# Performance work log

Hardware: AMD Instinct MI355X
Metric: run time of the kernel (lower is better)

The kernel has to match this reference:

```python
import jax, jax.numpy as jnp
import numpy as np

D = 2048      # input_dim
E = 16        # num_experts
H = 1024      # expert_units
K = 4         # k_top
B = 4096      # batch


def setup_inputs() -> dict:
    key = jax.random.key(0)
    ks = jax.random.split(key, 7)
    s1 = 1.0 / np.sqrt(D)
    s2 = 1.0 / np.sqrt(H)
    return {
        "x": jax.random.normal(ks[0], (B, D), dtype=jnp.float32),
        "W1": jax.random.uniform(ks[1], (E, D, H), jnp.float32, -s1, s1),
        "b1": jax.random.uniform(ks[2], (E, H), jnp.float32, -s1, s1),
        "W2": jax.random.uniform(ks[3], (E, H, D), jnp.float32, -s2, s2),
        "b2": jax.random.uniform(ks[4], (E, D), jnp.float32, -s2, s2),
        "Wr": jax.random.uniform(ks[5], (D, E), jnp.float32, -s1, s1),
        "br": jax.random.uniform(ks[6], (E,), jnp.float32, -s1, s1),
    }


def reference(x, W1, b1, W2, b2, Wr, br):
    # Router + top-k (torch.topk returns sorted descending; lax.top_k matches)
    logits = x @ Wr + br                          # [B, E]
    top_w, top_i = jax.lax.top_k(logits, K)       # [B, K]
    top_w = jax.nn.softmax(top_w, axis=1)

    # Dense all-expert MLP (eval mode: dropout is identity)
    h = jax.nn.relu(jnp.einsum('bd,edh->beh', x, W1) + b1)   # [B, E, H]
    expert_out = jnp.einsum('beh,ehd->bed', h, W2) + b2      # [B, E, D]

    # mask/detach trick: forward value is unchanged (identity in fwd)
    mask = jax.nn.one_hot(top_i, E, dtype=expert_out.dtype).sum(axis=1)  # [B, E]
    m = mask[:, :, None]
    expert_out = expert_out * m + jax.lax.stop_gradient(expert_out * (1.0 - m))

    # Gather top-k experts and combine
    sel = jnp.take_along_axis(expert_out, top_i[:, :, None], axis=1)    # [B, K, D]
    out = (sel * top_w[:, :, None]).sum(axis=1)
    return out + x
```

## Files before the change

kernel.cpp:

```cpp
#include <hip/hip_runtime.h>
#include <math.h>

#define D_   2048
#define E_   16
#define H_   1024
#define KSEL 4
#define B_   4096
#define CAP  4096

typedef short bf16x8_t __attribute__((ext_vector_type(8)));
typedef float f32x4_t  __attribute__((ext_vector_type(4)));

__device__ __forceinline__ unsigned short f2bf(float f) {
  unsigned u = __float_as_uint(f);
  u += 0x7FFFu + ((u >> 16) & 1u);
  return (unsigned short)(u >> 16);
}

__device__ __forceinline__ float bf2f(unsigned short h) {
  unsigned u = (unsigned)h << 16;
  return __uint_as_float(u);
}

__device__ __forceinline__ void gld16(const void* g, void* l) {
  __builtin_amdgcn_global_load_lds(
      (const __attribute__((address_space(1))) unsigned int*)g,
      (__attribute__((address_space(3))) unsigned int*)l, 16, 0, 0);
}

__global__ __launch_bounds__(256) void k_prepw(
    const float* __restrict__ Wr, float* __restrict__ wrT,
    const float* __restrict__ W1, unsigned short* __restrict__ W1t,
    const float* __restrict__ W2, unsigned short* __restrict__ W2t) {
  __shared__ float tile[64][65];
  int b = blockIdx.x;
  int w = threadIdx.x;
  if (b < 128) {
    int i = b * 256 + w;
    int d = i >> 4, e = i & 15;
    wrT[e * D_ + d] = Wr[i];
    return;
  }
  int g0 = (b - 128) * 2;
  const float* src[2]; unsigned short* dst[2];
  int RR[2], CC[2], r0t[2], c0t[2];
#pragma unroll
  for (int tt = 0; tt < 2; tt++) {
    int g = g0 + tt;
    if (g < 8192) {
      int e = g >> 9, rem = g & 511;
      src[tt] = W1 + (size_t)e * D_ * H_;
      dst[tt] = W1t + (size_t)e * D_ * H_;
      RR[tt] = 2048; CC[tt] = 1024;
      r0t[tt] = (rem >> 4) * 64; c0t[tt] = (rem & 15) * 64;
    } else {
      int g2 = g - 8192;
      int e = g2 >> 9, rem = g2 & 511;
      src[tt] = W2 + (size_t)e * D_ * H_;
      dst[tt] = W2t + (size_t)e * D_ * H_;
      RR[tt] = 1024; CC[tt] = 2048;
      r0t[tt] = (rem >> 5) * 64; c0t[tt] = (rem & 31) * 64;
    }
  }
  int cf4 = w & 15, rr = w >> 4;
  float4 v0[4], v1[4];
#pragma unroll
  for (int p = 0; p < 4; p++)
    v0[p] = *(const float4*)(src[0] + (size_t)(r0t[0] + p * 16 + rr) * CC[0] + c0t[0] + cf4 * 4);
#pragma unroll
  for (int p = 0; p < 4; p++)
    v1[p] = *(const float4*)(src[1] + (size_t)(r0t[1] + p * 16 + rr) * CC[1] + c0t[1] + cf4 * 4);
#pragma unroll
  for (int p = 0; p < 4; p++) {
    int r = p * 16 + rr;
    tile[r][cf4 * 4 + 0] = v0[p].x;
    tile[r][cf4 * 4 + 1] = v0[p].y;
    tile[r][cf4 * 4 + 2] = v0[p].z;
    tile[r][cf4 * 4 + 3] = v0[p].w;
  }
  __syncthreads();
#pragma unroll
  for (int it = 0; it < 8; it++) {
    int idx = it * 256 + w;
    int i = idx >> 5, rp = idx & 31;
    ushort2 v;
    v.x = f2bf(tile[2 * rp][i]);
    v.y = f2bf(tile[2 * rp + 1][i]);
    *(ushort2*)(dst[0] + (size_t)(c0t[0] + i) * RR[0] + r0t[0] + 2 * rp) = v;
  }
  __syncthreads();
#pragma unroll
  for (int p = 0; p < 4; p++) {
    int r = p * 16 + rr;
    tile[r][cf4 * 4 + 0] = v1[p].x;
    tile[r][cf4 * 4 + 1] = v1[p].y;
    tile[r][cf4 * 4 + 2] = v1[p].z;
    tile[r][cf4 * 4 + 3] = v1[p].w;
  }
  __syncthreads();
#pragma unroll
  for (int it = 0; it < 8; it++) {
    int idx = it * 256 + w;
    int i = idx >> 5, rp = idx & 31;
    ushort2 v;
    v.x = f2bf(tile[2 * rp][i]);
    v.y = f2bf(tile[2 * rp + 1][i]);
    *(ushort2*)(dst[1] + (size_t)(c0t[1] + i) * RR[1] + r0t[1] + 2 * rp) = v;
  }
}

__global__ __launch_bounds__(256) void k_router(
    const float* __restrict__ x, const float* __restrict__ wrT, const float* __restrict__ br,
    unsigned short* __restrict__ xb, int* __restrict__ tops, float* __restrict__ topw) {
  int wid = threadIdx.x >> 6, lane = threadIdx.x & 63;
  int t = blockIdx.x * 4 + wid;
  float acc[E_];
#pragma unroll
  for (int e = 0; e < E_; e++) acc[e] = 0.f;
  const float4* xr = (const float4*)(x + (size_t)t * D_);
  ushort4* xbw = (ushort4*)(xb + (size_t)t * D_);
#pragma unroll
  for (int j = 0; j < D_ / 256; j++) {
    float4 xv = xr[j * 64 + lane];
    ushort4 o;
    o.x = f2bf(xv.x); o.y = f2bf(xv.y); o.z = f2bf(xv.z); o.w = f2bf(xv.w);
    xbw[j * 64 + lane] = o;
#pragma unroll
    for (int e = 0; e < E_; e++) {
      float4 wv = ((const float4*)(wrT + (size_t)e * D_))[j * 64 + lane];
      acc[e] += xv.x * wv.x + xv.y * wv.y + xv.z * wv.z + xv.w * wv.w;
    }
  }
#pragma unroll
  for (int e = 0; e < E_; e++) {
    float v = acc[e];
    for (int m = 32; m >= 1; m >>= 1) v += __shfl_xor(v, m);
    acc[e] = v;
  }
  if (lane == 0) {
    float lg[E_];
#pragma unroll
    for (int e = 0; e < E_; e++) lg[e] = acc[e] + br[e];
    unsigned used = 0; int sel[KSEL]; float sv[KSEL];
    for (int k = 0; k < KSEL; k++) {
      float best = -1e30f; int bi = 0;
      for (int e = 0; e < E_; e++)
        if (!((used >> e) & 1u) && lg[e] > best) { best = lg[e]; bi = e; }
      used |= 1u << bi; sel[k] = bi; sv[k] = best;
    }
    float mx = sv[0], s = 0.f, w[KSEL];
    for (int k = 0; k < KSEL; k++) { w[k] = expf(sv[k] - mx); s += w[k]; }
    float inv = 1.f / s;
    int4 ti; float4 tw;
    ti.x = sel[0]; ti.y = sel[1]; ti.z = sel[2]; ti.w = sel[3];
    tw.x = w[0] * inv; tw.y = w[1] * inv; tw.z = w[2] * inv; tw.w = w[3] * inv;
    ((int4*)tops)[t] = ti;
    ((float4*)topw)[t] = tw;
  }
}

__global__ __launch_bounds__(256) void k_build(
    const int* __restrict__ tops, const float* __restrict__ topw,
    int* __restrict__ counts, int* __restrict__ ids, float* __restrict__ wts,
    int* __restrict__ inv) {
  int e = blockIdx.x;
  int tid = threadIdx.x, lane = tid & 63, wid = tid >> 6;
  __shared__ int wsum[4];
  __shared__ int red[4];
  int base = 0;
  int pre = 0;
  for (int c = 0; c < B_; c += 256) {
    int t = c + tid;
    int4 tk = ((const int4*)tops)[t];
    pre += (tk.x < e) + (tk.y < e) + (tk.z < e) + (tk.w < e);
    int k = -1;
    if (tk.x == e) k = 0; else if (tk.y == e) k = 1;
    else if (tk.z == e) k = 2; else if (tk.w == e) k = 3;
    unsigned long long mask = __ballot(k >= 0);
    int myoff = __popcll(mask & ((1ull << lane) - 1ull));
    if (lane == 0) wsum[wid] = __popcll(mask);
    __syncthreads();
    int woff = 0;
#pragma unroll
    for (int i = 0; i < 4; i++) if (i < wid) woff += wsum[i];
    int ctotal = wsum[0] + wsum[1] + wsum[2] + wsum[3];
    if (k >= 0) {
      int slot = base + woff + myoff;
      ids[e * CAP + slot] = t;
      wts[e * CAP + slot] = topw[t * 4 + k];
    }
    base += ctotal;
    __syncthreads();
  }
  if (tid == 0) counts[e] = base;
  for (int m = 32; m >= 1; m >>= 1) pre += __shfl_xor(pre, m);
  if (lane == 0) red[wid] = pre;
  __syncthreads();
  int offe = red[0] + red[1] + red[2] + red[3];
  for (int s = tid; s < base; s += 256) {
    int t = ids[e * CAP + s];
    int4 tk = ((const int4*)tops)[t];
    int k = (tk.x == e) ? 0 : (tk.y == e) ? 1 : (tk.z == e) ? 2 : 3;
    inv[t * 4 + k] = offe + s;
  }
}

__global__ __launch_bounds__(256) void k_gather(
    const float* __restrict__ x, const unsigned short* __restrict__ ybuf,
    const int* __restrict__ inv, float* __restrict__ out) {
  int t = blockIdx.x;
  int4 iv = ((const int4*)inv)[t];
  const ushort4* y0 = (const ushort4*)(ybuf + (size_t)iv.x * D_);
  const ushort4* y1 = (const ushort4*)(ybuf + (size_t)iv.y * D_);
  const ushort4* y2 = (const ushort4*)(ybuf + (size_t)iv.z * D_);
  const ushort4* y3 = (const ushort4*)(ybuf + (size_t)iv.w * D_);
  const float4* xr = (const float4*)(x + (size_t)t * D_);
  float4* orow = (float4*)(out + (size_t)t * D_);
#pragma unroll
  for (int i = threadIdx.x; i < D_ / 4; i += 256) {
    float4 v = xr[i];
    ushort4 a = y0[i], b = y1[i], c = y2[i], d = y3[i];
    v.x += bf2f(a.x) + bf2f(b.x) + bf2f(c.x) + bf2f(d.x);
    v.y += bf2f(a.y) + bf2f(b.y) + bf2f(c.y) + bf2f(d.y);
    v.z += bf2f(a.z) + bf2f(b.z) + bf2f(c.z) + bf2f(d.z);
    v.w += bf2f(a.w) + bf2f(b.w) + bf2f(c.w) + bf2f(d.w);
    orow[i] = v;
  }
}


__global__ __launch_bounds__(256, 3) void k_gemm1(
    const unsigned short* __restrict__ xb,
    const unsigned short* __restrict__ w1t,
    const float* __restrict__ b1,
    const int* __restrict__ ids, const int* __restrict__ counts,
    unsigned short* __restrict__ hbuf)
{
  __shared__ unsigned short As[128 * 64];
  __shared__ unsigned short Bs[128 * 64];
  const int NS = H_ / 128;
  int cnts[E_], offsv[E_], rowt[E_], cumt[E_];
  int s = 0, tcum = 0;
#pragma unroll
  for (int e = 0; e < E_; e++) {
    cnts[e] = counts[e];
    offsv[e] = s; s += cnts[e];
    rowt[e] = (cnts[e] + 127) >> 7;
    cumt[e] = tcum; tcum += rowt[e] * NS;
  }
  int totalTiles = tcum;
  int bswz = (blockIdx.x & 7) * (gridDim.x >> 3) + (blockIdx.x >> 3);
  if (bswz >= totalTiles) return;
  int tile = bswz;
  int tid = threadIdx.x, lane = tid & 63, wid = tid >> 6;
  int wr = wid >> 1, wc = wid & 1;
  int cr = lane >> 3, slot = lane & 7;
  int sw = (slot ^ cr) << 3;
  int hi = lane >> 4, cl = lane & 15;

  int e = 0;
  while (e < E_ - 1 && tile >= cumt[e + 1]) e++;
  int local = tile - cumt[e];
  int slab = local / rowt[e];
  int rt = local - slab * rowt[e];
  int n0 = slab << 7;
  int cnt = cnts[e];
  int r0 = rt << 7;

  const unsigned short* a_src[4];
  const unsigned short* b_src[4];
  const unsigned short* wbase = w1t + (size_t)e * H_ * D_;
#pragma unroll
  for (int i = 0; i < 4; i++) {
    int chunk = wid * 4 + i;
    int rr = r0 + chunk * 8 + cr;
    int rc = min(rr, cnt - 1);
    int tok = ids[e * CAP + rc];
    a_src[i] = xb + (size_t)tok * D_ + sw;
    b_src[i] = wbase + (size_t)(n0 + chunk * 8 + cr) * D_ + sw;
  }
  f32x4_t acc[4][4];
#pragma unroll
  for (int m = 0; m < 4; m++)
#pragma unroll
    for (int n = 0; n < 4; n++) acc[m][n] = (f32x4_t){0.f, 0.f, 0.f, 0.f};

  for (int kt = 0; kt < D_; kt += 64) {
#pragma unroll
    for (int i = 0; i < 4; i++) {
      gld16(a_src[i] + kt, As + (wid * 4 + i) * 512);
      gld16(b_src[i] + kt, Bs + (wid * 4 + i) * 512);
    }
    __syncthreads();
#pragma unroll
    for (int kb = 0; kb < 2; kb++) {
      bf16x8_t af[4], bfr[4];
#pragma unroll
      for (int m = 0; m < 4; m++) {
        int row = wr * 64 + m * 16 + (lane & 15);
        int ss = (kb * 4 + (lane >> 4)) ^ (row & 7);
        af[m] = *(const bf16x8_t*)(As + row * 64 + ss * 8);
      }
#pragma unroll
      for (int n = 0; n < 4; n++) {
        int row = wc * 64 + n * 16 + (lane & 15);
        int ss = (kb * 4 + (lane >> 4)) ^ (row & 7);
        bfr[n] = *(const bf16x8_t*)(Bs + row * 64 + ss * 8);
      }
#pragma unroll
      for (int m = 0; m < 4; m++)
#pragma unroll
        for (int n = 0; n < 4; n++)
          acc[m][n] = __builtin_amdgcn_mfma_f32_16x16x32_bf16(af[m], bfr[n], acc[m][n], 0, 0, 0);
    }
    __syncthreads();
  }
  int offe = offsv[e];
  float bias[4];
#pragma unroll
  for (int n = 0; n < 4; n++)
    bias[n] = b1[e * H_ + n0 + wc * 64 + n * 16 + cl];
#pragma unroll
  for (int m = 0; m < 4; m++)
#pragma unroll
    for (int j = 0; j < 4; j++) {
      int sr = r0 + wr * 64 + m * 16 + hi * 4 + j;
      if (sr < cnt) {
        size_t rowb = (size_t)(offe + sr) * H_;
#pragma unroll
        for (int n = 0; n < 4; n++) {
          int col = n0 + wc * 64 + n * 16 + cl;
          float v = acc[m][n][j] + bias[n];
          v = v > 0.f ? v : 0.f;
          hbuf[rowb + col] = f2bf(v);
        }
      }
    }
}

__global__ __launch_bounds__(256, 3) void k_gemm2(
    const unsigned short* __restrict__ hbuf,
    const unsigned short* __restrict__ w2t,
    const float* __restrict__ b2,
    const float* __restrict__ wts,
    const int* __restrict__ counts,
    unsigned short* __restrict__ ybuf)
{
  __shared__ unsigned short As[128 * 64];
  __shared__ unsigned short Bs[128 * 64];
  const int NS = D_ / 128;
  int cnts[E_], offsv[E_], rowt[E_], cumt[E_];
  int s = 0, tcum = 0;
#pragma unroll
  for (int e = 0; e < E_; e++) {
    cnts[e] = counts[e];
    offsv[e] = s; s += cnts[e];
    rowt[e] = (cnts[e] + 127) >> 7;
    cumt[e] = tcum; tcum += rowt[e] * NS;
  }
  int totalTiles = tcum;
  int bswz = (blockIdx.x & 7) * (gridDim.x >> 3) + (blockIdx.x >> 3);
  if (bswz >= totalTiles) return;
  int tile = bswz;
  int tid = threadIdx.x, lane = tid & 63, wid = tid >> 6;
  int wr = wid >> 1, wc = wid & 1;
  int cr = lane >> 3, slot = lane & 7;
  int sw = (slot ^ cr) << 3;
  int hi = lane >> 4, cl = lane & 15;

  int e = 0;
  while (e < E_ - 1 && tile >= cumt[e + 1]) e++;
  int local = tile - cumt[e];
  int slab = local / rowt[e];
  int rt = local - slab * rowt[e];
  int n0 = slab << 7;
  int cnt = cnts[e];
  int r0 = rt << 7;
  int offe = offsv[e];

  const unsigned short* a_src[4];
  const unsigned short* b_src[4];
  const unsigned short* wbase = w2t + (size_t)e * D_ * H_;
#pragma unroll
  for (int i = 0; i < 4; i++) {
    int chunk = wid * 4 + i;
    int rr = r0 + chunk * 8 + cr;
    int rc = min(rr, cnt - 1);
    a_src[i] = hbuf + (size_t)(offe + rc) * H_ + sw;
    b_src[i] = wbase + (size_t)(n0 + chunk * 8 + cr) * H_ + sw;
  }
  f32x4_t acc[4][4];
#pragma unroll
  for (int m = 0; m < 4; m++)
#pragma unroll
    for (int n = 0; n < 4; n++) acc[m][n] = (f32x4_t){0.f, 0.f, 0.f, 0.f};

  for (int kt = 0; kt < H_; kt += 64) {
#pragma unroll
    for (int i = 0; i < 4; i++) {
      gld16(a_src[i] + kt, As + (wid * 4 + i) * 512);
      gld16(b_src[i] + kt, Bs + (wid * 4 + i) * 512);
    }
    __syncthreads();
#pragma unroll
    for (int kb = 0; kb < 2; kb++) {
      bf16x8_t af[4], bfr[4];
#pragma unroll
      for (int m = 0; m < 4; m++) {
        int row = wr * 64 + m * 16 + (lane & 15);
        int ss = (kb * 4 + (lane >> 4)) ^ (row & 7);
        af[m] = *(const bf16x8_t*)(As + row * 64 + ss * 8);
      }
#pragma unroll
      for (int n = 0; n < 4; n++) {
        int row = wc * 64 + n * 16 + (lane & 15);
        int ss = (kb * 4 + (lane >> 4)) ^ (row & 7);
        bfr[n] = *(const bf16x8_t*)(Bs + row * 64 + ss * 8);
      }
#pragma unroll
      for (int m = 0; m < 4; m++)
#pragma unroll
        for (int n = 0; n < 4; n++)
          acc[m][n] = __builtin_amdgcn_mfma_f32_16x16x32_bf16(af[m], bfr[n], acc[m][n], 0, 0, 0);
    }
    __syncthreads();
  }
  float bias[4];
#pragma unroll
  for (int n = 0; n < 4; n++)
    bias[n] = b2[e * D_ + n0 + wc * 64 + n * 16 + cl];
#pragma unroll
  for (int m = 0; m < 4; m++)
#pragma unroll
    for (int j = 0; j < 4; j++) {
      int sr = r0 + wr * 64 + m * 16 + hi * 4 + j;
      if (sr < cnt) {
        float w = wts[e * CAP + sr];
        unsigned short* yrow = ybuf + (size_t)(offe + sr) * D_;
#pragma unroll
        for (int n = 0; n < 4; n++) {
          int col = n0 + wc * 64 + n * 16 + cl;
          yrow[col] = f2bf(w * (acc[m][n][j] + bias[n]));
        }
      }
    }
}

extern "C" void kernel_launch(void* const* d_in, const int* in_sizes, int n_in,
                              void* d_out, int out_size, void* d_ws, size_t ws_size,
                              hipStream_t stream) {
  const float* x  = (const float*)d_in[0];
  const float* W1 = (const float*)d_in[1];
  const float* b1 = (const float*)d_in[2];
  const float* W2 = (const float*)d_in[3];
  const float* b2 = (const float*)d_in[4];
  const float* Wr = (const float*)d_in[5];
  const float* br = (const float*)d_in[6];
  float* out = (float*)d_out;
  char* ws = (char*)d_ws;
  unsigned short* W1t  = (unsigned short*)(ws);
  unsigned short* ybuf = (unsigned short*)(ws);
  unsigned short* W2t  = (unsigned short*)(ws + 67108864);
  unsigned short* xb   = (unsigned short*)(ws + 134217728);
  unsigned short* hb   = (unsigned short*)(ws + 150994944);
  int*   ids    = (int*)  (ws + 184549376);
  float* wts    = (float*)(ws + 184811520);
  int*   counts = (int*)  (ws + 185073664);
  float* wrT    = (float*)(ws + 185073728);
  int*   tops   = (int*)  (ws + 185204800);
  float* topw   = (float*)(ws + 185270336);
  int*   inv    = (int*)  (ws + 185335872);

  k_prepw<<<8320, 256, 0, stream>>>(Wr, wrT, W1, W1t, W2, W2t);
  k_router<<<1024, 256, 0, stream>>>(x, wrT, br, xb, tops, topw);
  k_build<<<16, 256, 0, stream>>>(tops, topw, counts, ids, wts, inv);
  k_gemm1<<<1152, 256, 0, stream>>>(xb, W1t, b1, ids, counts, hb);
  k_gemm2<<<2304, 256, 0, stream>>>(hb, W2t, b2, wts, counts, ybuf);
  k_gather<<<4096, 256, 0, stream>>>(x, ybuf, inv, out);
}
```

Measured before the change: 387.9 us.

## Overlap W2 transpose/convert with first expert GEMM in one launch

Moves the W2 fp32→bf16 transpose out of the weight-prep kernel and interleaves it as extra blocks inside the gemm1 launch (8 GEMM blocks per 32-block chunk, the other 24 do transpose work). The aim is to hide the memory-bound W2 conversion behind the compute-bound first GEMM instead of running it serially. The shared memory is unioned between GEMM tiles and the transpose tile. The GEMM tile swizzle is now hardcoded (172 per group), which assumes a bound on the tile count, and the interleaving may hurt GEMM occupancy or its L2 locality.

```diff
diff --git a/kernel.cpp b/kernel.cpp
--- a/kernel.cpp
+++ b/kernel.cpp
@@ -28,10 +28,60 @@
       (__attribute__((address_space(3))) unsigned int*)l, 16, 0, 0);
 }
 
+__device__ __forceinline__ void trans2(
+    const float* src0, unsigned short* dst0, int R0, int C0, int r00, int c00,
+    const float* src1, unsigned short* dst1, int R1, int C1, int r01, int c01,
+    float (*tile)[65], int w) {
+  int cf4 = w & 15, rr = w >> 4;
+  float4 v0[4], v1[4];
+#pragma unroll
+  for (int p = 0; p < 4; p++)
+    v0[p] = *(const float4*)(src0 + (size_t)(r00 + p * 16 + rr) * C0 + c00 + cf4 * 4);
+#pragma unroll
+  for (int p = 0; p < 4; p++)
+    v1[p] = *(const float4*)(src1 + (size_t)(r01 + p * 16 + rr) * C1 + c01 + cf4 * 4);
+#pragma unroll
+  for (int p = 0; p < 4; p++) {
+    int r = p * 16 + rr;
+    tile[r][cf4 * 4 + 0] = v0[p].x;
+    tile[r][cf4 * 4 + 1] = v0[p].y;
+    tile[r][cf4 * 4 + 2] = v0[p].z;
+    tile[r][cf4 * 4 + 3] = v0[p].w;
+  }
+  __syncthreads();
+#pragma unroll
+  for (int it = 0; it < 8; it++) {
+    int idx = it * 256 + w;
+    int i = idx >> 5, rp = idx & 31;
+    ushort2 v;
+    v.x = f2bf(tile[2 * rp][i]);
+    v.y = f2bf(tile[2 * rp + 1][i]);
+    *(ushort2*)(dst0 + (size_t)(c00 + i) * R0 + r00 + 2 * rp) = v;
+  }
+  __syncthreads();
+#pragma unroll
+  for (int p = 0; p < 4; p++) {
+    int r = p * 16 + rr;
+    tile[r][cf4 * 4 + 0] = v1[p].x;
+    tile[r][cf4 * 4 + 1] = v1[p].y;
+    tile[r][cf4 * 4 + 2] = v1[p].z;
+    tile[r][cf4 * 4 + 3] = v1[p].w;
+  }
+  __syncthreads();
+#pragma unroll
+  for (int it = 0; it < 8; it++) {
+    int idx = it * 256 + w;
+    int i = idx >> 5, rp = idx & 31;
+    ushort2 v;
+    v.x = f2bf(tile[2 * rp][i]);
+    v.y = f2bf(tile[2 * rp + 1][i]);
+    *(ushort2*)(dst1 + (size_t)(c01 + i) * R1 + r01 + 2 * rp) = v;
+  }
+}
+
 __global__ __launch_bounds__(256) void k_prepw(
     const float* __restrict__ Wr, float* __restrict__ wrT,
-    const float* __restrict__ W1, unsigned short* __restrict__ W1t,
-    const float* __restrict__ W2, unsigned short* __restrict__ W2t) {
+    const float* __restrict__ W1, unsigned short* __restrict__ W1t) {
   __shared__ float tile[64][65];
   int b = blockIdx.x;
   int w = threadIdx.x;
@@ -42,71 +92,13 @@
     return;
   }
   int g0 = (b - 128) * 2;
-  const float* src[2]; unsigned short* dst[2];
-  int RR[2], CC[2], r0t[2], c0t[2];
-#pragma unroll
-  for (int tt = 0; tt < 2; tt++) {
-    int g = g0 + tt;
-    if (g < 8192) {
-      int e = g >> 9, rem = g & 511;
-      src[tt] = W1 + (size_t)e * D_ * H_;
-      dst[tt] = W1t + (size_t)e * D_ * H_;
-      RR[tt] = 2048; CC[tt] = 1024;
-      r0t[tt] = (rem >> 4) * 64; c0t[tt] = (rem & 15) * 64;
-    } else {
-      int g2 = g - 8192;
-      int e = g2 >> 9, rem = g2 & 511;
-      src[tt] = W2 + (size_t)e * D_ * H_;
-      dst[tt] = W2t + (size_t)e * D_ * H_;
-      RR[tt] = 1024; CC[tt] = 2048;
-      r0t[tt] = (rem >> 5) * 64; c0t[tt] = (rem & 31) * 64;
-    }
-  }
-  int cf4 = w & 15, rr = w >> 4;
-  float4 v0[4], v1[4];
-#pragma unroll
-  for (int p = 0; p < 4; p++)
-    v0[p] = *(const float4*)(src[0] + (size_t)(r0t[0] + p * 16 + rr) * CC[0] + c0t[0] + cf4 * 4);
-#pragma unroll
-  for (int p = 0; p < 4; p++)
-    v1[p] = *(const float4*)(src[1] + (size_t)(r0t[1] + p * 16 + rr) * CC[1] + c0t[1] + cf4 * 4);
-#pragma unroll
-  for (int p = 0; p < 4; p++) {
-    int r = p * 16 + rr;
-    tile[r][cf4 * 4 + 0] = v0[p].x;
-    tile[r][cf4 * 4 + 1] = v0[p].y;
-    tile[r][cf4 * 4 + 2] = v0[p].z;
-    tile[r][cf4 * 4 + 3] = v0[p].w;
-  }
-  __syncthreads();
-#pragma unroll
-  for (int it = 0; it < 8; it++) {
-    int idx = it * 256 + w;
-    int i = idx >> 5, rp = idx & 31;
-    ushort2 v;
-    v.x = f2bf(tile[2 * rp][i]);
-    v.y = f2bf(tile[2 * rp + 1][i]);
-    *(ushort2*)(dst[0] + (size_t)(c0t[0] + i) * RR[0] + r0t[0] + 2 * rp) = v;
-  }
-  __syncthreads();
-#pragma unroll
-  for (int p = 0; p < 4; p++) {
-    int r = p * 16 + rr;
-    tile[r][cf4 * 4 + 0] = v1[p].x;
-    tile[r][cf4 * 4 + 1] = v1[p].y;
-    tile[r][cf4 * 4 + 2] = v1[p].z;
-    tile[r][cf4 * 4 + 3] = v1[p].w;
-  }
-  __syncthreads();
-#pragma unroll
-  for (int it = 0; it < 8; it++) {
-    int idx = it * 256 + w;
-    int i = idx >> 5, rp = idx & 31;
-    ushort2 v;
-    v.x = f2bf(tile[2 * rp][i]);
-    v.y = f2bf(tile[2 * rp + 1][i]);
-    *(ushort2*)(dst[1] + (size_t)(c0t[1] + i) * RR[1] + r0t[1] + 2 * rp) = v;
-  }
+  int e0 = g0 >> 9, rem0 = g0 & 511;
+  int g1 = g0 + 1;
+  int e1 = g1 >> 9, rem1 = g1 & 511;
+  trans2(W1 + (size_t)e0 * D_ * H_, W1t + (size_t)e0 * D_ * H_, 2048, 1024,
+         (rem0 >> 4) * 64, (rem0 & 15) * 64,
+         W1 + (size_t)e1 * D_ * H_, W1t + (size_t)e1 * D_ * H_, 2048, 1024,
+         (rem1 >> 4) * 64, (rem1 & 15) * 64, tile, w);
 }
 
 __global__ __launch_bounds__(256) void k_router(
@@ -234,10 +226,31 @@
     const unsigned short* __restrict__ w1t,
     const float* __restrict__ b1,
     const int* __restrict__ ids, const int* __restrict__ counts,
-    unsigned short* __restrict__ hbuf)
+    unsigned short* __restrict__ hbuf,
+    const float* __restrict__ W2, unsigned short* __restrict__ W2t)
 {
-  __shared__ unsigned short As[128 * 64];
-  __shared__ unsigned short Bs[128 * 64];
+  __shared__ char smem[32768];
+  unsigned short* As = (unsigned short*)smem;
+  unsigned short* Bs = (unsigned short*)(smem + 16384);
+  int idx = blockIdx.x;
+  int chunkb = idx >> 5, off = idx & 31;
+  int w = threadIdx.x;
+  if (off >= 8) {
+    int tIdx = chunkb * 24 + (off - 8);
+    if (tIdx >= 4096) return;
+    float (*tile)[65] = (float(*)[65])smem;
+    int g0 = tIdx * 2;
+    int e0 = g0 >> 9, rem0 = g0 & 511;
+    int g1 = g0 + 1;
+    int e1 = g1 >> 9, rem1 = g1 & 511;
+    trans2(W2 + (size_t)e0 * D_ * H_, W2t + (size_t)e0 * D_ * H_, 1024, 2048,
+           (rem0 >> 5) * 64, (rem0 & 31) * 64,
+           W2 + (size_t)e1 * D_ * H_, W2t + (size_t)e1 * D_ * H_, 1024, 2048,
+           (rem1 >> 5) * 64, (rem1 & 31) * 64, tile, w);
+    return;
+  }
+  int gemmIdx = chunkb * 8 + off;
+  int tile = (gemmIdx & 7) * 172 + (gemmIdx >> 3);
   const int NS = H_ / 128;
   int cnts[E_], offsv[E_], rowt[E_], cumt[E_];
   int s = 0, tcum = 0;
@@ -248,10 +261,7 @@
     rowt[e] = (cnts[e] + 127) >> 7;
     cumt[e] = tcum; tcum += rowt[e] * NS;
   }
-  int totalTiles = tcum;
-  int bswz = (blockIdx.x & 7) * (gridDim.x >> 3) + (blockIdx.x >> 3);
-  if (bswz >= totalTiles) return;
-  int tile = bswz;
+  if (tile >= tcum) return;
   int tid = threadIdx.x, lane = tid & 63, wid = tid >> 6;
   int wr = wid >> 1, wc = wid & 1;
   int cr = lane >> 3, slot = lane & 7;
@@ -471,10 +481,10 @@
   float* topw   = (float*)(ws + 185270336);
   int*   inv    = (int*)  (ws + 185335872);
 
-  k_prepw<<<8320, 256, 0, stream>>>(Wr, wrT, W1, W1t, W2, W2t);
+  k_prepw<<<4224, 256, 0, stream>>>(Wr, wrT, W1, W1t);
   k_router<<<1024, 256, 0, stream>>>(x, wrT, br, xb, tops, topw);
   k_build<<<16, 256, 0, stream>>>(tops, topw, counts, ids, wts, inv);
-  k_gemm1<<<1152, 256, 0, stream>>>(xb, W1t, b1, ids, counts, hb);
+  k_gemm1<<<5504, 256, 0, stream>>>(xb, W1t, b1, ids, counts, hb, W2, W2t);
   k_gemm2<<<2304, 256, 0, stream>>>(hb, W2t, b2, wts, counts, ybuf);
   k_gather<<<4096, 256, 0, stream>>>(x, ybuf, inv, out);
 }
```

New measurement: 548.3 us. 1.41x slower.
